# Kernel optimization log

Measured on AMD Instinct MI355X. Metric: run time of the kernel, lower is better.

Reference implementation:

```python
import jax, jax.numpy as jnp
import numpy as np

G = 250000   # number of graphs
NPG = 4      # nodes per graph (3 jets + 1 muon)
H = 16       # hidden dim (32/2)
MH = 64      # mlp hidden (128/2)
LN_EPS = 1e-5


def setup_inputs() -> dict:
    key = jax.random.key(0)
    ks = jax.random.split(key, 16)
    N = G * NPG
    # fully connected directed edges within each 4-node graph (12 per graph)
    pairs = np.array([(i, j) for i in range(NPG) for j in range(NPG) if i != j], dtype=np.int64)
    off = (np.arange(G, dtype=np.int64) * NPG)[:, None]
    src = (off + pairs[None, :, 0].repeat(G, 0) if False else off + pairs[:, 0][None, :]).ravel()
    tgt = (off + pairs[:, 1][None, :]).ravel()
    edge_index = jnp.asarray(np.stack([src, tgt]))
    E = src.shape[0]
    type_id = jnp.asarray(np.tile(np.array([0, 0, 0, 1], dtype=np.int64), G))
    batch = jnp.asarray(np.repeat(np.arange(G, dtype=np.int64), NPG))

    def w(k, shape):
        return (jax.random.normal(k, shape, jnp.float32) * 0.1)

    return dict(
        x=jax.random.normal(ks[0], (N, 5), jnp.float32),
        edge_attr=jax.random.normal(ks[1], (E, 4), jnp.float32),
        je_w1=w(ks[2], (5, H)), je_b1=jnp.zeros((H,), jnp.float32),
        je_w2=w(ks[3], (H, H)), je_b2=jnp.zeros((H,), jnp.float32),
        mu_w1=w(ks[4], (5, H)), mu_b1=jnp.zeros((H,), jnp.float32),
        mu_w2=w(ks[5], (H, H)), mu_b2=jnp.zeros((H,), jnp.float32),
        lin1_w=w(ks[6], (4, H)), lin1_b=jnp.zeros((H,), jnp.float32),
        m1_w1=w(ks[7], (H, MH)), m1_b1=jnp.zeros((MH,), jnp.float32),
        m1_w2=w(ks[8], (MH, H)), m1_b2=jnp.zeros((H,), jnp.float32),
        lin2_w=w(ks[9], (4, H)), lin2_b=jnp.zeros((H,), jnp.float32),
        m2_w1=w(ks[10], (H, MH)), m2_b1=jnp.zeros((MH,), jnp.float32),
        m2_w2=w(ks[11], (MH, H)), m2_b2=jnp.zeros((H,), jnp.float32),
        fc_w1=w(ks[12], (2 * H, MH)), fc_b1=jnp.zeros((MH,), jnp.float32),
        fc_w2=w(ks[13], (MH, 1)), fc_b2=jnp.zeros((1,), jnp.float32),
        type_id=type_id, edge_index=edge_index, batch=batch, num_graphs=G,
    )


def _ln(z):
    m = z.mean(-1, keepdims=True)
    v = z.var(-1, keepdims=True)
    return (z - m) / jnp.sqrt(v + LN_EPS)


def _mlp(z, w1, b1, w2, b2):
    return jax.nn.relu(z @ w1 + b1) @ w2 + b2


def _gine(h, edge_attr, src, tgt, lw, lb, w1, b1, w2, b2, n_nodes):
    # message: relu(x_j + Lin(edge_attr)); aggregate: scatter-sum at target; eps=0
    msg = jax.nn.relu(h[src] + edge_attr @ lw + lb)          # [E, H]
    agg = jax.ops.segment_sum(msg, tgt, num_segments=n_nodes)  # [N, H]
    return _mlp(h + agg, w1, b1, w2, b2)


def reference(x, edge_attr,
              je_w1, je_b1, je_w2, je_b2,
              mu_w1, mu_b1, mu_w2, mu_b2,
              lin1_w, lin1_b, m1_w1, m1_b1, m1_w2, m1_b2,
              lin2_w, lin2_b, m2_w1, m2_b1, m2_w2, m2_b2,
              fc_w1, fc_b1, fc_w2, fc_b2,
              type_id, edge_index, batch, num_graphs):
    n_nodes = x.shape[0]
    src, tgt = edge_index[0], edge_index[1]
    # heterogeneous encoders (masks are disjoint and cover all nodes)
    h_jet = _mlp(x, je_w1, je_b1, je_w2, je_b2)
    h_mu = _mlp(x, mu_w1, mu_b1, mu_w2, mu_b2)
    h = jnp.where((type_id == 0)[:, None], h_jet, h_mu)      # [N, H]
    # two GINEConv + layernorm + relu blocks
    h = _gine(h, edge_attr, src, tgt, lin1_w, lin1_b, m1_w1, m1_b1, m1_w2, m1_b2, n_nodes)
    h = jax.nn.relu(_ln(h))
    h = _gine(h, edge_attr, src, tgt, lin2_w, lin2_b, m2_w1, m2_b1, m2_w2, m2_b2, n_nodes)
    h = jax.nn.relu(_ln(h))
    # pooling per graph
    counts = jax.ops.segment_sum(jnp.ones((n_nodes,), h.dtype), batch, num_segments=num_graphs)
    x_mean = jax.ops.segment_sum(h, batch, num_segments=num_graphs) / counts[:, None]
    x_max = jax.ops.segment_max(h, batch, num_segments=num_graphs)
    g = _ln(jnp.concatenate([x_mean, x_max], axis=1))        # [G, 2H]
    return _mlp(g, fc_w1, fc_b1, fc_w2, fc_b2)               # [G, 1]
```

## Files before the change

kernel.cpp:

```cpp
#include <hip/hip_runtime.h>

#define H 16
#define MH 64
#define LN_EPS 1e-5f


typedef _Float16 f16;
typedef f16 f16x2 __attribute__((ext_vector_type(2)));
typedef f16 f16x4 __attribute__((ext_vector_type(4)));
typedef __fp16 fp16x2 __attribute__((ext_vector_type(2)));
typedef float f32x4 __attribute__((ext_vector_type(4)));

#define MFMA16(a, b, c) __builtin_amdgcn_mfma_f32_16x16x16f16((a), (b), (c), 0, 0, 0)

__device__ __forceinline__ void split4v(float a0, float a1, float a2, float a3,
                                        f16x4& hi, f16x4& lo)
{
    fp16x2 h01 = __builtin_amdgcn_cvt_pkrtz(a0, a1);
    fp16x2 h23 = __builtin_amdgcn_cvt_pkrtz(a2, a3);
    fp16x2 l01 = __builtin_amdgcn_cvt_pkrtz(a0 - (float)h01[0], a1 - (float)h01[1]);
    fp16x2 l23 = __builtin_amdgcn_cvt_pkrtz(a2 - (float)h23[0], a3 - (float)h23[1]);
    const f16x2 H01 = __builtin_bit_cast(f16x2, h01);
    const f16x2 H23 = __builtin_bit_cast(f16x2, h23);
    const f16x2 L01 = __builtin_bit_cast(f16x2, l01);
    const f16x2 L23 = __builtin_bit_cast(f16x2, l23);
    hi = __builtin_shufflevector(H01, H23, 0, 1, 2, 3);
    lo = __builtin_shufflevector(L01, L23, 0, 1, 2, 3);
}

__device__ __forceinline__ void gine_block(f32x4& hT, const int g,
    const float* __restrict__ edge_attr,
    const f16x4* __restrict__ wsb,
    const float* __restrict__ cstb,
    const int p, const int qg, const int t, const int lane)
{
    const f32x4 zero4 = {0.f, 0.f, 0.f, 0.f};

    float uv0 = hT[0], uv1 = hT[1], uv2 = hT[2], uv3 = hT[3];
    {
        const f32x4 lb4 = *(const f32x4*)&cstb[64 + 4 * qg];
        const f32x4 lw0 = *(const f32x4*)&cstb[0  + 4 * qg];
        const f32x4 lw1 = *(const f32x4*)&cstb[16 + 4 * qg];
        const f32x4 lw2 = *(const f32x4*)&cstb[32 + 4 * qg];
        const f32x4 lw3 = *(const f32x4*)&cstb[48 + 4 * qg];
#pragma unroll
        for (int m = 1; m <= 3; ++m) {
            const int s  = t ^ m;
            const int el = s * 3 + (t < s ? t : t - 1);
            const f32x4 e = *(const f32x4*)(edge_attr + (g * 12 + el) * 4);
            const float h0 = __shfl_xor(hT[0], m, 64);
            const float h1 = __shfl_xor(hT[1], m, 64);
            const float h2 = __shfl_xor(hT[2], m, 64);
            const float h3 = __shfl_xor(hT[3], m, 64);
            float l0 = lb4[0], l1 = lb4[1], l2 = lb4[2], l3 = lb4[3];
            l0 = fmaf(e[0], lw0[0], l0); l1 = fmaf(e[0], lw0[1], l1);
            l2 = fmaf(e[0], lw0[2], l2); l3 = fmaf(e[0], lw0[3], l3);
            l0 = fmaf(e[1], lw1[0], l0); l1 = fmaf(e[1], lw1[1], l1);
            l2 = fmaf(e[1], lw1[2], l2); l3 = fmaf(e[1], lw1[3], l3);
            l0 = fmaf(e[2], lw2[0], l0); l1 = fmaf(e[2], lw2[1], l1);
            l2 = fmaf(e[2], lw2[2], l2); l3 = fmaf(e[2], lw2[3], l3);
            l0 = fmaf(e[3], lw3[0], l0); l1 = fmaf(e[3], lw3[1], l1);
            l2 = fmaf(e[3], lw3[2], l2); l3 = fmaf(e[3], lw3[3], l3);
            uv0 += fmaxf(h0 + l0, 0.f); uv1 += fmaxf(h1 + l1, 0.f);
            uv2 += fmaxf(h2 + l2, 0.f); uv3 += fmaxf(h3 + l3, 0.f);
        }
    }
    f16x4 uh, ul;
    split4v(uv0, uv1, uv2, uv3, uh, ul);

    f32x4 aA = zero4, aB = zero4;
    auto mt_step = [&](int mt, f32x4& acc) {
        const f16x4 a1h = wsb[mt * 64 + lane];
        const f16x4 a1l = wsb[(4 + mt) * 64 + lane];
        f32x4 z = zero4;
        z = MFMA16(a1h, uh, z);
        z = MFMA16(a1h, ul, z);
        z = MFMA16(a1l, uh, z);
        const f32x4 b1v = *(const f32x4*)&cstb[80 + 16 * mt + 4 * qg];
        const float s0 = fmaxf(fmaf(z[0], 0.015625f, b1v[0]), 0.f);
        const float s1 = fmaxf(fmaf(z[1], 0.015625f, b1v[1]), 0.f);
        const float s2 = fmaxf(fmaf(z[2], 0.015625f, b1v[2]), 0.f);
        const float s3 = fmaxf(fmaf(z[3], 0.015625f, b1v[3]), 0.f);
        f16x4 sh, sl;
        split4v(s0, s1, s2, s3, sh, sl);
        const f16x4 a2h = wsb[(8 + mt) * 64 + lane];
        const f16x4 a2l = wsb[(12 + mt) * 64 + lane];
        acc = MFMA16(a2h, sh, acc);
        acc = MFMA16(a2h, sl, acc);
        acc = MFMA16(a2l, sh, acc);
    };
    mt_step(0, aA); mt_step(1, aB); mt_step(2, aA); mt_step(3, aB);

    const f32x4 b2q = *(const f32x4*)&cstb[144 + 4 * qg];
    float o0 = fmaf(aA[0] + aB[0], 0.015625f, b2q[0]);
    float o1 = fmaf(aA[1] + aB[1], 0.015625f, b2q[1]);
    float o2 = fmaf(aA[2] + aB[2], 0.015625f, b2q[2]);
    float o3 = fmaf(aA[3] + aB[3], 0.015625f, b2q[3]);

    float sum = o0 + o1 + o2 + o3;
    sum += __shfl_xor(sum, 16, 64);
    sum += __shfl_xor(sum, 32, 64);
    const float mean = sum * (1.f / 16.f);
    const float d0 = o0 - mean, d1 = o1 - mean, d2 = o2 - mean, d3 = o3 - mean;
    float q = fmaf(d0, d0, fmaf(d1, d1, fmaf(d2, d2, d3 * d3)));
    q += __shfl_xor(q, 16, 64);
    q += __shfl_xor(q, 32, 64);
    const float rr = rsqrtf(q * (1.f / 16.f) + LN_EPS);
    hT[0] = fmaxf(d0 * rr, 0.f); hT[1] = fmaxf(d1 * rr, 0.f);
    hT[2] = fmaxf(d2 * rr, 0.f); hT[3] = fmaxf(d3 * rr, 0.f);
}

__global__ __launch_bounds__(256) void gnn_npl_kernel(
    const float* __restrict__ x,
    const float* __restrict__ edge_attr,
    const float* __restrict__ je_w1, const float* __restrict__ je_b1,
    const float* __restrict__ je_w2, const float* __restrict__ je_b2,
    const float* __restrict__ mu_w1, const float* __restrict__ mu_b1,
    const float* __restrict__ mu_w2, const float* __restrict__ mu_b2,
    const float* __restrict__ l1w, const float* __restrict__ l1b,
    const float* __restrict__ m1w1, const float* __restrict__ m1b1,
    const float* __restrict__ m1w2, const float* __restrict__ m1b2,
    const float* __restrict__ l2w, const float* __restrict__ l2b,
    const float* __restrict__ m2w1, const float* __restrict__ m2b1,
    const float* __restrict__ m2w2, const float* __restrict__ m2b2,
    const float* __restrict__ fcw1, const float* __restrict__ fcb1,
    const float* __restrict__ fcw2, const float* __restrict__ fcb2,
    float* __restrict__ out, int nG)
{
    __shared__ __align__(16) char smem[16384 + 1280];
    f16x4* ws   = (f16x4*)smem;
    float* cst  = (float*)(smem + 16384);
    f16x4* fcf  = (f16x4*)smem;
    float* cbuf = (float*)(smem + 8192);

    const int tIdx = threadIdx.x;
    const int lane = tIdx & 63;
    const int wv   = tIdx >> 6;
    const int p    = lane & 15;
    const int qg   = lane >> 4;
    const int t    = p & 3;
    int g = blockIdx.x * 16 + 4 * wv + (p >> 2);
    if (g >= nG) g = nG - 1;

    const f32x4 zero4 = {0.f, 0.f, 0.f, 0.f};

    if (wv < 2) {
        const float* w1 = wv ? m2w1 : m1w1;
        const float* w2 = wv ? m2w2 : m1w2;
        f16x4* wb = ws + wv * 16 * 64;
#pragma unroll
        for (int s = 0; s < 4; ++s) {
            f16x4 hF, lF;
            split4v(64.f * w1[(4 * qg + 0) * MH + 16 * s + p],
                    64.f * w1[(4 * qg + 1) * MH + 16 * s + p],
                    64.f * w1[(4 * qg + 2) * MH + 16 * s + p],
                    64.f * w1[(4 * qg + 3) * MH + 16 * s + p], hF, lF);
            wb[s * 64 + lane] = hF;
            wb[(4 + s) * 64 + lane] = lF;
        }
#pragma unroll
        for (int s = 0; s < 4; ++s) {
            f16x4 hF, lF;
            split4v(64.f * w2[(16 * s + 4 * qg + 0) * H + p],
                    64.f * w2[(16 * s + 4 * qg + 1) * H + p],
                    64.f * w2[(16 * s + 4 * qg + 2) * H + p],
                    64.f * w2[(16 * s + 4 * qg + 3) * H + p], hF, lF);
            wb[(8 + s) * 64 + lane] = hF;
            wb[(12 + s) * 64 + lane] = lF;
        }
    } else if (lane < 40) {
        const int b = wv - 2;
        const float* W  = b ? l2w  : l1w;
        const float* LB = b ? l2b  : l1b;
        const float* B1 = b ? m2b1 : m1b1;
        const float* B2 = b ? m2b2 : m1b2;
        const int i4 = 4 * lane;
        const float* src = (i4 < 64)  ? (W  + i4)
                         : (i4 < 80)  ? (LB + (i4 - 64))
                         : (i4 < 144) ? (B1 + (i4 - 80))
                         :              (B2 + (i4 - 144));
        *(f32x4*)&cst[b * 160 + i4] = *(const f32x4*)src;
    }

    const int node = g * 4 + t;
    float x0 = 0.f, x1 = 0.f, x2 = 0.f, x3 = 0.f;
    if (qg == 0) {
        const float* xp = x + node * 5;
        x0 = xp[0]; x1 = xp[1]; x2 = xp[2]; x3 = xp[3];
    } else if (qg == 1) {
        x0 = x[node * 5 + 4];
    }
    f16x4 xbh, xbl;
    split4v(x0, x1, x2, x3, xbh, xbl);

    auto enc_path = [&](const float* w1, const float* b1,
                        const float* w2, const float* b2) -> f32x4 {
        float wj[4];
#pragma unroll
        for (int j = 0; j < 4; ++j) {
            const int k = 4 * qg + j;
            wj[j] = (k < 5) ? 64.f * w1[k * H + p] : 0.f;
        }
        f16x4 a1h, a1l;
        split4v(wj[0], wj[1], wj[2], wj[3], a1h, a1l);
        f32x4 z = zero4;
        z = MFMA16(a1h, xbh, z); z = MFMA16(a1h, xbl, z); z = MFMA16(a1l, xbh, z);
        const f32x4 b14 = *(const f32x4*)(b1 + 4 * qg);
        const float s0 = fmaxf(fmaf(z[0], 0.015625f, b14[0]), 0.f);
        const float s1 = fmaxf(fmaf(z[1], 0.015625f, b14[1]), 0.f);
        const float s2 = fmaxf(fmaf(z[2], 0.015625f, b14[2]), 0.f);
        const float s3 = fmaxf(fmaf(z[3], 0.015625f, b14[3]), 0.f);
        f16x4 th, tl;
        split4v(s0, s1, s2, s3, th, tl);
#pragma unroll
        for (int j = 0; j < 4; ++j) wj[j] = 64.f * w2[(4 * qg + j) * H + p];
        f16x4 a2h, a2l;
        split4v(wj[0], wj[1], wj[2], wj[3], a2h, a2l);
        f32x4 o = zero4;
        o = MFMA16(a2h, th, o); o = MFMA16(a2h, tl, o); o = MFMA16(a2l, th, o);
        const f32x4 b24 = *(const f32x4*)(b2 + 4 * qg);
        f32x4 hv;
#pragma unroll
        for (int r = 0; r < 4; ++r) hv[r] = fmaf(o[r], 0.015625f, b24[r]);
        return hv;
    };
    const f32x4 hj = enc_path(je_w1, je_b1, je_w2, je_b2);
    const f32x4 hm = enc_path(mu_w1, mu_b1, mu_w2, mu_b2);
    f32x4 hT;
#pragma unroll
    for (int r = 0; r < 4; ++r) hT[r] = (t == 3) ? hm[r] : hj[r];

    __syncthreads();

    gine_block(hT, g, edge_attr, ws,           cst,       p, qg, t, lane);
    gine_block(hT, g, edge_attr, ws + 16 * 64, cst + 160, p, qg, t, lane);

    __syncthreads();

    if (wv >= 2) {
        const int base_mt = (wv - 2) * 2;
#pragma unroll
        for (int i = 0; i < 2; ++i) {
            const int mt = base_mt + i;
#pragma unroll
            for (int kt = 0; kt < 2; ++kt) {
                f16x4 hF, lF;
                split4v(64.f * fcw1[(16 * kt + 4 * qg + 0) * MH + 16 * mt + p],
                        64.f * fcw1[(16 * kt + 4 * qg + 1) * MH + 16 * mt + p],
                        64.f * fcw1[(16 * kt + 4 * qg + 2) * MH + 16 * mt + p],
                        64.f * fcw1[(16 * kt + 4 * qg + 3) * MH + 16 * mt + p],
                        hF, lF);
                fcf[((mt * 2 + kt) * 2 + 0) * 64 + lane] = hF;
                fcf[((mt * 2 + kt) * 2 + 1) * 64 + lane] = lF;
            }
        }
    }

    {
        float mn[4], mx[4];
#pragma unroll
        for (int r = 0; r < 4; ++r) {
            float sm = hT[r], mv = hT[r];
            sm += __shfl_xor(sm, 1, 64); mv = fmaxf(mv, __shfl_xor(mv, 1, 64));
            sm += __shfl_xor(sm, 2, 64); mv = fmaxf(mv, __shfl_xor(mv, 2, 64));
            mn[r] = sm * 0.25f; mx[r] = mv;
        }
        float S = 0.f;
#pragma unroll
        for (int r = 0; r < 4; ++r) S += mn[r] + mx[r];
        S += __shfl_xor(S, 16, 64);
        S += __shfl_xor(S, 32, 64);
        const float mean = S * (1.f / 32.f);
        float q = 0.f;
#pragma unroll
        for (int r = 0; r < 4; ++r) {
            const float dn = mn[r] - mean, dx = mx[r] - mean;
            q = fmaf(dn, dn, q); q = fmaf(dx, dx, q);
        }
        q += __shfl_xor(q, 16, 64);
        q += __shfl_xor(q, 32, 64);
        const float rr = rsqrtf(q * (1.f / 32.f) + LN_EPS);
        if (t == 0) {
            f32x4 cn, cx;
#pragma unroll
            for (int r = 0; r < 4; ++r) {
                cn[r] = (mn[r] - mean) * rr;
                cx[r] = (mx[r] - mean) * rr;
            }
            const int row = 4 * wv + (p >> 2);
            *(f32x4*)(cbuf + row * 36 + 4 * qg)      = cn;
            *(f32x4*)(cbuf + row * 36 + 16 + 4 * qg) = cx;
        }
    }
    __syncthreads();

    if (wv == 0) {
        const int gb = p;
        f16x4 bh[2], bl[2];
#pragma unroll
        for (int kt = 0; kt < 2; ++kt) {
            const f32x4 cv = *(const f32x4*)(cbuf + gb * 36 + 16 * kt + 4 * qg);
            split4v(cv[0], cv[1], cv[2], cv[3], bh[kt], bl[kt]);
        }
        float acc = 0.f;
#pragma unroll
        for (int mt = 0; mt < 4; ++mt) {
            f32x4 z = zero4;
#pragma unroll
            for (int kt = 0; kt < 2; ++kt) {
                const f16x4 ah = fcf[((mt * 2 + kt) * 2 + 0) * 64 + lane];
                const f16x4 al = fcf[((mt * 2 + kt) * 2 + 1) * 64 + lane];
                z = MFMA16(ah, bh[kt], z);
                z = MFMA16(ah, bl[kt], z);
                z = MFMA16(al, bh[kt], z);
            }
            const f32x4 b1v = *(const f32x4*)(fcb1 + 16 * mt + 4 * qg);
            const f32x4 w2v = *(const f32x4*)(fcw2 + 16 * mt + 4 * qg);
#pragma unroll
            for (int r = 0; r < 4; ++r)
                acc = fmaf(fmaxf(fmaf(z[r], 0.015625f, b1v[r]), 0.f), w2v[r], acc);
        }
        acc += __shfl_xor(acc, 16, 64);
        acc += __shfl_xor(acc, 32, 64);
        if (lane < 16) {
            const int gq = blockIdx.x * 16 + lane;
            if (gq < nG) out[gq] = acc + fcb2[0];
        }
    }
}

extern "C" void kernel_launch(void* const* d_in, const int* in_sizes, int n_in,
                              void* d_out, int out_size, void* d_ws, size_t ws_size,
                              hipStream_t stream) {
    const float* x         = (const float*)d_in[0];
    const float* edge_attr = (const float*)d_in[1];
    const float* je_w1 = (const float*)d_in[2];
    const float* je_b1 = (const float*)d_in[3];
    const float* je_w2 = (const float*)d_in[4];
    const float* je_b2 = (const float*)d_in[5];
    const float* mu_w1 = (const float*)d_in[6];
    const float* mu_b1 = (const float*)d_in[7];
    const float* mu_w2 = (const float*)d_in[8];
    const float* mu_b2 = (const float*)d_in[9];
    const float* l1w   = (const float*)d_in[10];
    const float* l1b   = (const float*)d_in[11];
    const float* m1w1  = (const float*)d_in[12];
    const float* m1b1  = (const float*)d_in[13];
    const float* m1w2  = (const float*)d_in[14];
    const float* m1b2  = (const float*)d_in[15];
    const float* l2w   = (const float*)d_in[16];
    const float* l2b   = (const float*)d_in[17];
    const float* m2w1  = (const float*)d_in[18];
    const float* m2b1  = (const float*)d_in[19];
    const float* m2w2  = (const float*)d_in[20];
    const float* m2b2  = (const float*)d_in[21];
    const float* fcw1  = (const float*)d_in[22];
    const float* fcb1  = (const float*)d_in[23];
    const float* fcw2  = (const float*)d_in[24];
    const float* fcb2  = (const float*)d_in[25];

    const int nG = out_size;
    const int blocks = (nG + 15) / 16;
    gnn_npl_kernel<<<blocks, 256, 0, stream>>>(
        x, edge_attr,
        je_w1, je_b1, je_w2, je_b2,
        mu_w1, mu_b1, mu_w2, mu_b2,
        l1w, l1b, m1w1, m1b1, m1w2, m1b2,
        l2w, l2b, m2w1, m2b1, m2w2, m2b2,
        fcw1, fcb1, fcw2, fcb2,
        (float*)d_out, nG);
}
```

Baseline: 252.8 us.

## Double block size, stage encoder and FC weights in LDS once per block

```diff
diff --git a/kernel.cpp b/kernel.cpp
--- a/kernel.cpp
+++ b/kernel.cpp
@@ -28,11 +28,10 @@
     lo = __builtin_shufflevector(L01, L23, 0, 1, 2, 3);
 }
 
-__device__ __forceinline__ void gine_block(f32x4& hT, const int g,
-    const float* __restrict__ edge_attr,
+__device__ __forceinline__ void gine_block(f32x4& hT, const f32x4 ea[3],
     const f16x4* __restrict__ wsb,
     const float* __restrict__ cstb,
-    const int p, const int qg, const int t, const int lane)
+    const int qg, const int lane)
 {
     const f32x4 zero4 = {0.f, 0.f, 0.f, 0.f};
 
@@ -45,9 +44,7 @@
         const f32x4 lw3 = *(const f32x4*)&cstb[48 + 4 * qg];
 #pragma unroll
         for (int m = 1; m <= 3; ++m) {
-            const int s  = t ^ m;
-            const int el = s * 3 + (t < s ? t : t - 1);
-            const f32x4 e = *(const f32x4*)(edge_attr + (g * 12 + el) * 4);
+            const f32x4 e = ea[m - 1];
             const float h0 = __shfl_xor(hT[0], m, 64);
             const float h1 = __shfl_xor(hT[1], m, 64);
             const float h2 = __shfl_xor(hT[2], m, 64);
@@ -92,10 +89,10 @@
     mt_step(0, aA); mt_step(1, aB); mt_step(2, aA); mt_step(3, aB);
 
     const f32x4 b2q = *(const f32x4*)&cstb[144 + 4 * qg];
-    float o0 = fmaf(aA[0] + aB[0], 0.015625f, b2q[0]);
-    float o1 = fmaf(aA[1] + aB[1], 0.015625f, b2q[1]);
-    float o2 = fmaf(aA[2] + aB[2], 0.015625f, b2q[2]);
-    float o3 = fmaf(aA[3] + aB[3], 0.015625f, b2q[3]);
+    const float o0 = fmaf(aA[0] + aB[0], 0.015625f, b2q[0]);
+    const float o1 = fmaf(aA[1] + aB[1], 0.015625f, b2q[1]);
+    const float o2 = fmaf(aA[2] + aB[2], 0.015625f, b2q[2]);
+    const float o3 = fmaf(aA[3] + aB[3], 0.015625f, b2q[3]);
 
     float sum = o0 + o1 + o2 + o3;
     sum += __shfl_xor(sum, 16, 64);
@@ -110,7 +107,7 @@
     hT[2] = fmaxf(d2 * rr, 0.f); hT[3] = fmaxf(d3 * rr, 0.f);
 }
 
-__global__ __launch_bounds__(256) void gnn_npl_kernel(
+__global__ __launch_bounds__(512) void gnn_npl_kernel(
     const float* __restrict__ x,
     const float* __restrict__ edge_attr,
     const float* __restrict__ je_w1, const float* __restrict__ je_b1,
@@ -127,11 +124,13 @@
     const float* __restrict__ fcw2, const float* __restrict__ fcb2,
     float* __restrict__ out, int nG)
 {
-    __shared__ __align__(16) char smem[16384 + 1280];
+    __shared__ __align__(16) char smem[30208];
     f16x4* ws   = (f16x4*)smem;
-    float* cst  = (float*)(smem + 16384);
-    f16x4* fcf  = (f16x4*)smem;
-    float* cbuf = (float*)(smem + 8192);
+    f16x4* fcf  = (f16x4*)(smem + 16384);
+    f16x4* encf = (f16x4*)(smem + 24576);
+    float* cst  = (float*)(smem + 28672);
+    float* encb = (float*)(smem + 29952);
+    float* cbuf = (float*)smem;
 
     const int tIdx = threadIdx.x;
     const int lane = tIdx & 63;
@@ -139,7 +138,7 @@
     const int p    = lane & 15;
     const int qg   = lane >> 4;
     const int t    = p & 3;
-    int g = blockIdx.x * 16 + 4 * wv + (p >> 2);
+    int g = blockIdx.x * 32 + 4 * wv + (p >> 2);
     if (g >= nG) g = nG - 1;
 
     const f32x4 zero4 = {0.f, 0.f, 0.f, 0.f};
@@ -168,80 +167,9 @@
             wb[(8 + s) * 64 + lane] = hF;
             wb[(12 + s) * 64 + lane] = lF;
         }
-    } else if (lane < 40) {
-        const int b = wv - 2;
-        const float* W  = b ? l2w  : l1w;
-        const float* LB = b ? l2b  : l1b;
-        const float* B1 = b ? m2b1 : m1b1;
-        const float* B2 = b ? m2b2 : m1b2;
-        const int i4 = 4 * lane;
-        const float* src = (i4 < 64)  ? (W  + i4)
-                         : (i4 < 80)  ? (LB + (i4 - 64))
-                         : (i4 < 144) ? (B1 + (i4 - 80))
-                         :              (B2 + (i4 - 144));
-        *(f32x4*)&cst[b * 160 + i4] = *(const f32x4*)src;
-    }
-
-    const int node = g * 4 + t;
-    float x0 = 0.f, x1 = 0.f, x2 = 0.f, x3 = 0.f;
-    if (qg == 0) {
-        const float* xp = x + node * 5;
-        x0 = xp[0]; x1 = xp[1]; x2 = xp[2]; x3 = xp[3];
-    } else if (qg == 1) {
-        x0 = x[node * 5 + 4];
-    }
-    f16x4 xbh, xbl;
-    split4v(x0, x1, x2, x3, xbh, xbl);
-
-    auto enc_path = [&](const float* w1, const float* b1,
-                        const float* w2, const float* b2) -> f32x4 {
-        float wj[4];
-#pragma unroll
-        for (int j = 0; j < 4; ++j) {
-            const int k = 4 * qg + j;
-            wj[j] = (k < 5) ? 64.f * w1[k * H + p] : 0.f;
-        }
-        f16x4 a1h, a1l;
-        split4v(wj[0], wj[1], wj[2], wj[3], a1h, a1l);
-        f32x4 z = zero4;
-        z = MFMA16(a1h, xbh, z); z = MFMA16(a1h, xbl, z); z = MFMA16(a1l, xbh, z);
-        const f32x4 b14 = *(const f32x4*)(b1 + 4 * qg);
-        const float s0 = fmaxf(fmaf(z[0], 0.015625f, b14[0]), 0.f);
-        const float s1 = fmaxf(fmaf(z[1], 0.015625f, b14[1]), 0.f);
-        const float s2 = fmaxf(fmaf(z[2], 0.015625f, b14[2]), 0.f);
-        const float s3 = fmaxf(fmaf(z[3], 0.015625f, b14[3]), 0.f);
-        f16x4 th, tl;
-        split4v(s0, s1, s2, s3, th, tl);
-#pragma unroll
-        for (int j = 0; j < 4; ++j) wj[j] = 64.f * w2[(4 * qg + j) * H + p];
-        f16x4 a2h, a2l;
-        split4v(wj[0], wj[1], wj[2], wj[3], a2h, a2l);
-        f32x4 o = zero4;
-        o = MFMA16(a2h, th, o); o = MFMA16(a2h, tl, o); o = MFMA16(a2l, th, o);
-        const f32x4 b24 = *(const f32x4*)(b2 + 4 * qg);
-        f32x4 hv;
-#pragma unroll
-        for (int r = 0; r < 4; ++r) hv[r] = fmaf(o[r], 0.015625f, b24[r]);
-        return hv;
-    };
-    const f32x4 hj = enc_path(je_w1, je_b1, je_w2, je_b2);
-    const f32x4 hm = enc_path(mu_w1, mu_b1, mu_w2, mu_b2);
-    f32x4 hT;
-#pragma unroll
-    for (int r = 0; r < 4; ++r) hT[r] = (t == 3) ? hm[r] : hj[r];
-
-    __syncthreads();
-
-    gine_block(hT, g, edge_attr, ws,           cst,       p, qg, t, lane);
-    gine_block(hT, g, edge_attr, ws + 16 * 64, cst + 160, p, qg, t, lane);
-
-    __syncthreads();
-
-    if (wv >= 2) {
-        const int base_mt = (wv - 2) * 2;
-#pragma unroll
-        for (int i = 0; i < 2; ++i) {
-            const int mt = base_mt + i;
+    } else if (wv == 2) {
+#pragma unroll
+        for (int mt = 0; mt < 4; ++mt) {
 #pragma unroll
             for (int kt = 0; kt < 2; ++kt) {
                 f16x4 hF, lF;
@@ -254,7 +182,107 @@
                 fcf[((mt * 2 + kt) * 2 + 1) * 64 + lane] = lF;
             }
         }
-    }
+    } else if (wv == 3) {
+        float wj[4];
+        f16x4 hF, lF;
+#pragma unroll
+        for (int j = 0; j < 4; ++j) {
+            const int k = 4 * qg + j;
+            wj[j] = (k < 5) ? 64.f * je_w1[k * H + p] : 0.f;
+        }
+        split4v(wj[0], wj[1], wj[2], wj[3], hF, lF);
+        encf[0 * 64 + lane] = hF; encf[1 * 64 + lane] = lF;
+#pragma unroll
+        for (int j = 0; j < 4; ++j) wj[j] = 64.f * je_w2[(4 * qg + j) * H + p];
+        split4v(wj[0], wj[1], wj[2], wj[3], hF, lF);
+        encf[2 * 64 + lane] = hF; encf[3 * 64 + lane] = lF;
+#pragma unroll
+        for (int j = 0; j < 4; ++j) {
+            const int k = 4 * qg + j;
+            wj[j] = (k < 5) ? 64.f * mu_w1[k * H + p] : 0.f;
+        }
+        split4v(wj[0], wj[1], wj[2], wj[3], hF, lF);
+        encf[4 * 64 + lane] = hF; encf[5 * 64 + lane] = lF;
+#pragma unroll
+        for (int j = 0; j < 4; ++j) wj[j] = 64.f * mu_w2[(4 * qg + j) * H + p];
+        split4v(wj[0], wj[1], wj[2], wj[3], hF, lF);
+        encf[6 * 64 + lane] = hF; encf[7 * 64 + lane] = lF;
+    } else if (wv == 4 || wv == 5) {
+        if (lane < 40) {
+            const int b = wv - 4;
+            const float* W  = b ? l2w  : l1w;
+            const float* LB = b ? l2b  : l1b;
+            const float* B1 = b ? m2b1 : m1b1;
+            const float* B2 = b ? m2b2 : m1b2;
+            const int i4 = 4 * lane;
+            const float* src = (i4 < 64)  ? (W  + i4)
+                             : (i4 < 80)  ? (LB + (i4 - 64))
+                             : (i4 < 144) ? (B1 + (i4 - 80))
+                             :              (B2 + (i4 - 144));
+            *(f32x4*)&cst[b * 160 + i4] = *(const f32x4*)src;
+        }
+    } else if (wv == 6) {
+        if (lane < 16) {
+            encb[lane]      = je_b1[lane];
+            encb[16 + lane] = mu_b1[lane];
+            encb[32 + lane] = je_b2[lane];
+            encb[48 + lane] = mu_b2[lane];
+        }
+    }
+
+    const int node = g * 4 + t;
+    float x0 = 0.f, x1 = 0.f, x2 = 0.f, x3 = 0.f;
+    if (qg == 0) {
+        const float* xp = x + node * 5;
+        x0 = xp[0]; x1 = xp[1]; x2 = xp[2]; x3 = xp[3];
+    } else if (qg == 1) {
+        x0 = x[node * 5 + 4];
+    }
+    f16x4 xbh, xbl;
+    split4v(x0, x1, x2, x3, xbh, xbl);
+
+    f32x4 ea[3];
+#pragma unroll
+    for (int m = 1; m <= 3; ++m) {
+        const int s  = t ^ m;
+        const int el = s * 3 + (t < s ? t : t - 1);
+        ea[m - 1] = *(const f32x4*)(edge_attr + (g * 12 + el) * 4);
+    }
+
+    __syncthreads();
+
+    auto enc_path = [&](int fb, int bo1, int bo2) -> f32x4 {
+        const f16x4 a1h = encf[(fb + 0) * 64 + lane];
+        const f16x4 a1l = encf[(fb + 1) * 64 + lane];
+        f32x4 z = zero4;
+        z = MFMA16(a1h, xbh, z); z = MFMA16(a1h, xbl, z); z = MFMA16(a1l, xbh, z);
+        const f32x4 b14 = *(const f32x4*)&encb[bo1 + 4 * qg];
+        const float s0 = fmaxf(fmaf(z[0], 0.015625f, b14[0]), 0.f);
+        const float s1 = fmaxf(fmaf(z[1], 0.015625f, b14[1]), 0.f);
+        const float s2 = fmaxf(fmaf(z[2], 0.015625f, b14[2]), 0.f);
+        const float s3 = fmaxf(fmaf(z[3], 0.015625f, b14[3]), 0.f);
+        f16x4 th, tl;
+        split4v(s0, s1, s2, s3, th, tl);
+        const f16x4 a2h = encf[(fb + 2) * 64 + lane];
+        const f16x4 a2l = encf[(fb + 3) * 64 + lane];
+        f32x4 o = zero4;
+        o = MFMA16(a2h, th, o); o = MFMA16(a2h, tl, o); o = MFMA16(a2l, th, o);
+        const f32x4 b24 = *(const f32x4*)&encb[bo2 + 4 * qg];
+        f32x4 hv;
+#pragma unroll
+        for (int r = 0; r < 4; ++r) hv[r] = fmaf(o[r], 0.015625f, b24[r]);
+        return hv;
+    };
+    const f32x4 hj = enc_path(0, 0, 32);
+    const f32x4 hm = enc_path(4, 16, 48);
+    f32x4 hT;
+#pragma unroll
+    for (int r = 0; r < 4; ++r) hT[r] = (t == 3) ? hm[r] : hj[r];
+
+    gine_block(hT, ea, ws,           cst,       qg, lane);
+    gine_block(hT, ea, ws + 16 * 64, cst + 160, qg, lane);
+
+    __syncthreads();
 
     {
         float mn[4], mx[4];
@@ -294,12 +322,12 @@
     }
     __syncthreads();
 
-    if (wv == 0) {
-        const int gb = p;
+    if (wv < 2) {
+        const int row = 16 * wv + p;
         f16x4 bh[2], bl[2];
 #pragma unroll
         for (int kt = 0; kt < 2; ++kt) {
-            const f32x4 cv = *(const f32x4*)(cbuf + gb * 36 + 16 * kt + 4 * qg);
+            const f32x4 cv = *(const f32x4*)(cbuf + row * 36 + 16 * kt + 4 * qg);
             split4v(cv[0], cv[1], cv[2], cv[3], bh[kt], bl[kt]);
         }
         float acc = 0.f;
@@ -323,7 +351,7 @@
         acc += __shfl_xor(acc, 16, 64);
         acc += __shfl_xor(acc, 32, 64);
         if (lane < 16) {
-            const int gq = blockIdx.x * 16 + lane;
+            const int gq = blockIdx.x * 32 + 16 * wv + lane;
             if (gq < nG) out[gq] = acc + fcb2[0];
         }
     }
@@ -360,8 +388,8 @@
     const float* fcb2  = (const float*)d_in[25];
 
     const int nG = out_size;
-    const int blocks = (nG + 15) / 16;
-    gnn_npl_kernel<<<blocks, 256, 0, stream>>>(
+    const int blocks = (nG + 31) / 32;
+    gnn_npl_kernel<<<blocks, 512, 0, stream>>>(
         x, edge_attr,
         je_w1, je_b1, je_w2, je_b2,
         mu_w1, mu_b1, mu_w2, mu_b2,
```

Result: faster. 232.6 us (-8.0%).
